# Performance work log

Measured on AMD Instinct MI355X. Metric: run time of the kernel, lower is better.

## Reference

```python
import jax, jax.numpy as jnp
import numpy as np

N, H = 8192, 256
TOP_K = 16          # k = min(top_k, N-1)
TEMPERATURE = 1.0
NEG_SLOPE = 0.2
NUM_SECTORS = 11


def setup_inputs() -> dict:
    key = jax.random.key(0)
    kE, kW, ka, ks, kA = jax.random.split(key, 5)
    embeddings = jax.random.normal(kE, (N, H), dtype=jnp.float32)
    # xavier-uniform-like scale for W (nn.Linear, bias=False)
    lim = float(np.sqrt(6.0 / (H + H)))
    W = jax.random.uniform(kW, (H, H), dtype=jnp.float32, minval=-lim, maxval=lim)
    # a ~ Normal(0, 1/sqrt(2H))
    a = jax.random.normal(ka, (2 * H,), dtype=jnp.float32) * (1.0 / np.sqrt(2 * H))
    sector_ids = jax.random.randint(ks, (N,), 0, NUM_SECTORS, dtype=jnp.int32)
    active_mask = jax.random.randint(kA, (N,), 0, 2, dtype=jnp.int32).astype(bool)
    return {"embeddings": embeddings, "W": W, "a": a,
            "sector_ids": sector_ids, "active_mask": active_mask}


def reference(embeddings, W, a, sector_ids, active_mask):
    # h = W(embeddings)  (torch Linear: x @ W.T)
    h = embeddings @ W.T                                   # [N, H]
    # attention[i,j] = leaky_relu(a . [h_i, h_j]) = leaky_relu(a1.h_i + a2.h_j)
    # (decomposition of the concat+matmul; same math, avoids O(N^2*2H) tensor)
    a1, a2 = a[:H], a[H:]
    s_i = h @ a1                                           # [N]
    s_j = h @ a2                                           # [N]
    att = jax.nn.leaky_relu(s_i[:, None] + s_j[None, :], NEG_SLOPE) / TEMPERATURE
    # combined mask: active pairs AND same sector
    mask = (active_mask[:, None] & active_mask[None, :]) \
           & (sector_ids[:, None] == sector_ids[None, :])  # [N, N]
    att = jnp.where(mask, att, -jnp.inf)
    k = min(TOP_K, N - 1)
    topk_values, topk_indices = jax.lax.top_k(att, k)      # [N, k] each
    valid = jnp.isfinite(topk_values)                      # invalid = masked-out slots
    # dense padded representation of (edge_index, edge_weight):
    # src = topk_indices, dst = row index, weight = topk_values where valid
    edge_weight = jnp.where(valid, topk_values, 0.0)
    return edge_weight, topk_indices, valid
```

## Files before the change

### kernel.cpp

```cpp
#include <hip/hip_runtime.h>

#define N 8192
#define H 256
#define TOPK 16
#define NSEC 11
#define NEG_SLOPE 0.2
#define NBLK 32
#define RPB (N / NBLK)
#define IDX_SENT 0x7fffffff

__device__ __forceinline__ bool better(double av, int ai, double bv, int bi) {
    return (av > bv) || (av == bv && ai < bi);
}

__global__ __launch_bounds__(1024) void fused_v_s(
    const float* __restrict__ E, const float* __restrict__ W,
    const float* __restrict__ a, const int* __restrict__ sec,
    const int* __restrict__ act,
    float* __restrict__ s1f, float* __restrict__ s2f,
    double* __restrict__ candV, int* __restrict__ candI,
    int* __restrict__ cnts)
{
    __shared__ double part1[4][256];
    __shared__ double part2[4][256];
    __shared__ double sv1[H];
    __shared__ double sv2[H];
    __shared__ double s2loc[RPB];

    int t = threadIdx.x;
    int blk = blockIdx.x;
    int lane = t & 63;
    int w = t >> 6;

    {
        int k = t & 255;
        int g = t >> 8;
        double acc1 = 0.0, acc2 = 0.0;
        for (int j = g * 64; j < (g + 1) * 64; ++j) {
            double wv = (double)W[j * H + k];
            acc1 += wv * (double)a[j];
            acc2 += wv * (double)a[H + j];
        }
        part1[g][k] = acc1;
        part2[g][k] = acc2;
    }
    __syncthreads();
    if (t < 256) {
        sv1[t] = part1[0][t] + part1[1][t] + part1[2][t] + part1[3][t];
        sv2[t] = part2[0][t] + part2[1][t] + part2[2][t] + part2[3][t];
    }
    __syncthreads();

    for (int q = 0; q < RPB / 16; ++q) {
        int r_loc = w + 16 * q;
        int row = blk * RPB + r_loc;
        const float4* Erow = (const float4*)(E + (size_t)row * H);
        float4 e = Erow[lane];
        int base = lane * 4;
        double acc1 = (double)e.x * sv1[base + 0] + (double)e.y * sv1[base + 1] +
                      (double)e.z * sv1[base + 2] + (double)e.w * sv1[base + 3];
        double acc2 = (double)e.x * sv2[base + 0] + (double)e.y * sv2[base + 1] +
                      (double)e.z * sv2[base + 2] + (double)e.w * sv2[base + 3];
        for (int o = 32; o > 0; o >>= 1) {
            acc1 += __shfl_down(acc1, o);
            acc2 += __shfl_down(acc2, o);
        }
        if (lane == 0) {
            s1f[row] = (float)acc1;
            s2f[row] = (float)acc2;
            s2loc[r_loc] = acc2;
        }
    }
    __syncthreads();

    if (w < NSEC) {
        int c = w;
        double cv[4];
        int ci[4];
        int count = 0;
        for (int p = 0; p < 4; ++p) {
            int r_loc = p * 64 + lane;
            int j = blk * RPB + r_loc;
            bool pred = (act[j] != 0) && (sec[j] == c);
            cv[p] = pred ? s2loc[r_loc] : -INFINITY;
            ci[p] = pred ? j : IDX_SENT;
            count += __popcll(__ballot(pred));
        }

        for (int r = 0; r < TOPK; ++r) {
            double bv = cv[0];
            int bi = ci[0];
            for (int p = 1; p < 4; ++p)
                if (better(cv[p], ci[p], bv, bi)) { bv = cv[p]; bi = ci[p]; }
            for (int o = 32; o > 0; o >>= 1) {
                double ov = __shfl_xor(bv, o);
                int oi = __shfl_xor(bi, o);
                if (better(ov, oi, bv, bi)) { bv = ov; bi = oi; }
            }
            if (bi != IDX_SENT) {
                for (int p = 0; p < 4; ++p)
                    if (ci[p] == bi) { cv[p] = -INFINITY; ci[p] = IDX_SENT; }
            }
            if (lane == 0) {
                candV[(c * NBLK + blk) * TOPK + r] = bv;
                candI[(c * NBLK + blk) * TOPK + r] = bi;
            }
        }
        if (lane == 0) cnts[c * NBLK + blk] = count;
    }
}

__global__ __launch_bounds__(64) void merge_topk(
    const double* __restrict__ candV, const int* __restrict__ candI,
    const int* __restrict__ cnts, const int* __restrict__ sec,
    const int* __restrict__ act,
    int* __restrict__ top_idx, int* __restrict__ fill_idx,
    int* __restrict__ m_out)
{
    int c = blockIdx.x;
    int lane = threadIdx.x;
    bool has = (lane < NBLK);

    const double* mybV = candV + (size_t)(c * NBLK + (has ? lane : 0)) * TOPK;
    const int* mybI = candI + (size_t)(c * NBLK + (has ? lane : 0)) * TOPK;

    double v0 = has ? mybV[0] : -INFINITY;
    int i0 = has ? mybI[0] : IDX_SENT;
    double v1 = has ? mybV[1] : -INFINITY;
    int i1 = has ? mybI[1] : IDX_SENT;
    int h = 0;

    for (int r = 0; r < TOPK; ++r) {
        double bv = v0;
        int bi = i0;
        for (int o = 32; o > 0; o >>= 1) {
            double ov = __shfl_xor(bv, o);
            int oi = __shfl_xor(bi, o);
            if (better(ov, oi, bv, bi)) { bv = ov; bi = oi; }
        }
        bool win = has && (i0 == bi) && (v0 == bv || (i0 == IDX_SENT));
        if (win) {
            ++h;
            v0 = v1;
            i0 = i1;
            if (h + 1 < TOPK) {
                v1 = mybV[h + 1];
                i1 = mybI[h + 1];
            } else {
                v1 = -INFINITY;
                i1 = IDX_SENT;
            }
        }
        if (lane == 0) top_idx[c * TOPK + r] = (bi == IDX_SENT) ? -1 : bi;
    }

    int cl = has ? cnts[c * NBLK + lane] : 0;
    for (int o = 32; o > 0; o >>= 1) cl += __shfl_xor(cl, o);
    if (lane == 0) m_out[c] = (cl < TOPK) ? cl : TOPK;

    int cnt2 = 0;
    for (int basej = 0; basej < N && cnt2 < TOPK; basej += 64) {
        int j = basej + lane;
        bool fail = !((act[j] != 0) && (sec[j] == c));
        unsigned long long mask = __ballot(fail);
        if (fail) {
            int rank = cnt2 + __popcll(mask & ((1ull << lane) - 1));
            if (rank < TOPK) fill_idx[c * TOPK + rank] = j;
        }
        cnt2 += __popcll(mask);
    }
}

__global__ __launch_bounds__(256) void write_out(const float* __restrict__ s1f,
                                                 const float* __restrict__ s2f,
                                                 const int* __restrict__ sec,
                                                 const int* __restrict__ act,
                                                 const int* __restrict__ top_idx,
                                                 const int* __restrict__ fill_idx,
                                                 const int* __restrict__ m_arr,
                                                 float* __restrict__ out) {
    int gid = blockIdx.x * 256 + threadIdx.x;
    int i = gid >> 4;
    int slot = gid & 15;

    float wgt = 0.0f;
    float fidx;
    float fvalid = 0.0f;

    if (act[i] == 0) {
        fidx = (float)slot;
    } else {
        int c = sec[i];
        int m = m_arr[c];
        if (slot < m) {
            int j = top_idx[c * TOPK + slot];
            double x = (double)s1f[i] + (double)s2f[j];
            double attv = (x >= 0.0) ? x : NEG_SLOPE * x;
            wgt = (float)attv;
            fvalid = 1.0f;
            fidx = (float)j;
        } else {
            fidx = (float)fill_idx[c * TOPK + (slot - m)];
        }
    }

    out[gid] = wgt;
    out[N * TOPK + gid] = fidx;
    out[2 * N * TOPK + gid] = fvalid;
}

extern "C" void kernel_launch(void* const* d_in, const int* in_sizes, int n_in,
                              void* d_out, int out_size, void* d_ws, size_t ws_size,
                              hipStream_t stream) {
    const float* E = (const float*)d_in[0];
    const float* W = (const float*)d_in[1];
    const float* a = (const float*)d_in[2];
    const int* sec = (const int*)d_in[3];
    const int* act = (const int*)d_in[4];

    char* ws = (char*)d_ws;
    double* candV = (double*)ws;
    float* s1f = (float*)(candV + NSEC * NBLK * TOPK);
    float* s2f = s1f + N;
    int* candI = (int*)(s2f + N);
    int* cnts = candI + NSEC * NBLK * TOPK;
    int* top_idx = cnts + NSEC * NBLK;
    int* fill_idx = top_idx + NSEC * TOPK;
    int* m_arr = fill_idx + NSEC * TOPK;

    float* out = (float*)d_out;

    hipLaunchKernelGGL(fused_v_s, dim3(NBLK), dim3(1024), 0, stream,
                       E, W, a, sec, act, s1f, s2f, candV, candI, cnts);
    hipLaunchKernelGGL(merge_topk, dim3(NSEC), dim3(64), 0, stream,
                       candV, candI, cnts, sec, act, top_idx, fill_idx, m_arr);
    hipLaunchKernelGGL(write_out, dim3((N * TOPK) / 256), dim3(256), 0, stream,
                       s1f, s2f, sec, act, top_idx, fill_idx, m_arr, out);
}
```

Measured before the change: 117.4 us.

## Fuse all stages into one cooperative kernel with grid syncs and per-sector compaction

New measurement: 226.7 us. 1.93x slower.

```diff
diff --git a/kernel.cpp b/kernel.cpp
--- a/kernel.cpp
+++ b/kernel.cpp
@@ -1,31 +1,38 @@
 #include <hip/hip_runtime.h>
+#include <hip/hip_cooperative_groups.h>
+
+namespace cg = cooperative_groups;
 
 #define N 8192
 #define H 256
 #define TOPK 16
 #define NSEC 11
 #define NEG_SLOPE 0.2
-#define NBLK 32
-#define RPB (N / NBLK)
+#define NB 256
+#define NT 256
+#define RPB (N / NB)
+#define CAP 1024
 #define IDX_SENT 0x7fffffff
 
 __device__ __forceinline__ bool better(double av, int ai, double bv, int bi) {
     return (av > bv) || (av == bv && ai < bi);
 }
 
-__global__ __launch_bounds__(1024) void fused_v_s(
+__global__ __launch_bounds__(NT) void fused_all(
     const float* __restrict__ E, const float* __restrict__ W,
     const float* __restrict__ a, const int* __restrict__ sec,
     const int* __restrict__ act,
-    float* __restrict__ s1f, float* __restrict__ s2f,
-    double* __restrict__ candV, int* __restrict__ candI,
-    int* __restrict__ cnts)
+    float* __restrict__ s1f, double* __restrict__ s2g,
+    int* __restrict__ top_idx, int* __restrict__ fill_idx,
+    int* __restrict__ m_arr, float* __restrict__ out)
 {
-    __shared__ double part1[4][256];
-    __shared__ double part2[4][256];
+    cg::grid_group grid = cg::this_grid();
+
     __shared__ double sv1[H];
     __shared__ double sv2[H];
-    __shared__ double s2loc[RPB];
+    __shared__ double kv[CAP];
+    __shared__ int ki[CAP];
+    __shared__ int s_cnt;
 
     int t = threadIdx.x;
     int blk = blockIdx.x;
@@ -33,26 +40,19 @@
     int w = t >> 6;
 
     {
-        int k = t & 255;
-        int g = t >> 8;
         double acc1 = 0.0, acc2 = 0.0;
-        for (int j = g * 64; j < (g + 1) * 64; ++j) {
-            double wv = (double)W[j * H + k];
+        for (int j = 0; j < H; ++j) {
+            double wv = (double)W[j * H + t];
             acc1 += wv * (double)a[j];
             acc2 += wv * (double)a[H + j];
         }
-        part1[g][k] = acc1;
-        part2[g][k] = acc2;
+        sv1[t] = acc1;
+        sv2[t] = acc2;
     }
     __syncthreads();
-    if (t < 256) {
-        sv1[t] = part1[0][t] + part1[1][t] + part1[2][t] + part1[3][t];
-        sv2[t] = part2[0][t] + part2[1][t] + part2[2][t] + part2[3][t];
-    }
-    __syncthreads();
-
-    for (int q = 0; q < RPB / 16; ++q) {
-        int r_loc = w + 16 * q;
+
+    for (int q = 0; q < RPB / 4; ++q) {
+        int r_loc = w + 4 * q;
         int row = blk * RPB + r_loc;
         const float4* Erow = (const float4*)(E + (size_t)row * H);
         float4 e = Erow[lane];
@@ -67,146 +67,158 @@
         }
         if (lane == 0) {
             s1f[row] = (float)acc1;
-            s2f[row] = (float)acc2;
-            s2loc[r_loc] = acc2;
-        }
-    }
-    __syncthreads();
-
-    if (w < NSEC) {
-        int c = w;
-        double cv[4];
-        int ci[4];
-        int count = 0;
-        for (int p = 0; p < 4; ++p) {
-            int r_loc = p * 64 + lane;
-            int j = blk * RPB + r_loc;
+            s2g[row] = acc2;
+        }
+    }
+
+    grid.sync();
+
+    if (blk < NSEC) {
+        int c = blk;
+        if (t == 0) s_cnt = 0;
+        __syncthreads();
+
+        for (int j = t; j < N; j += NT) {
             bool pred = (act[j] != 0) && (sec[j] == c);
-            cv[p] = pred ? s2loc[r_loc] : -INFINITY;
-            ci[p] = pred ? j : IDX_SENT;
-            count += __popcll(__ballot(pred));
-        }
-
-        for (int r = 0; r < TOPK; ++r) {
-            double bv = cv[0];
-            int bi = ci[0];
-            for (int p = 1; p < 4; ++p)
-                if (better(cv[p], ci[p], bv, bi)) { bv = cv[p]; bi = ci[p]; }
-            for (int o = 32; o > 0; o >>= 1) {
-                double ov = __shfl_xor(bv, o);
-                int oi = __shfl_xor(bi, o);
-                if (better(ov, oi, bv, bi)) { bv = ov; bi = oi; }
-            }
-            if (bi != IDX_SENT) {
-                for (int p = 0; p < 4; ++p)
-                    if (ci[p] == bi) { cv[p] = -INFINITY; ci[p] = IDX_SENT; }
-            }
-            if (lane == 0) {
-                candV[(c * NBLK + blk) * TOPK + r] = bv;
-                candI[(c * NBLK + blk) * TOPK + r] = bi;
-            }
-        }
-        if (lane == 0) cnts[c * NBLK + blk] = count;
-    }
-}
-
-__global__ __launch_bounds__(64) void merge_topk(
-    const double* __restrict__ candV, const int* __restrict__ candI,
-    const int* __restrict__ cnts, const int* __restrict__ sec,
-    const int* __restrict__ act,
-    int* __restrict__ top_idx, int* __restrict__ fill_idx,
-    int* __restrict__ m_out)
-{
-    int c = blockIdx.x;
-    int lane = threadIdx.x;
-    bool has = (lane < NBLK);
-
-    const double* mybV = candV + (size_t)(c * NBLK + (has ? lane : 0)) * TOPK;
-    const int* mybI = candI + (size_t)(c * NBLK + (has ? lane : 0)) * TOPK;
-
-    double v0 = has ? mybV[0] : -INFINITY;
-    int i0 = has ? mybI[0] : IDX_SENT;
-    double v1 = has ? mybV[1] : -INFINITY;
-    int i1 = has ? mybI[1] : IDX_SENT;
-    int h = 0;
-
-    for (int r = 0; r < TOPK; ++r) {
-        double bv = v0;
-        int bi = i0;
-        for (int o = 32; o > 0; o >>= 1) {
-            double ov = __shfl_xor(bv, o);
-            int oi = __shfl_xor(bi, o);
-            if (better(ov, oi, bv, bi)) { bv = ov; bi = oi; }
-        }
-        bool win = has && (i0 == bi) && (v0 == bv || (i0 == IDX_SENT));
-        if (win) {
-            ++h;
-            v0 = v1;
-            i0 = i1;
-            if (h + 1 < TOPK) {
-                v1 = mybV[h + 1];
-                i1 = mybI[h + 1];
+            unsigned long long mask = __ballot(pred);
+            int nact = __popcll(mask);
+            if (nact > 0) {
+                int leader = (int)__ffsll(mask) - 1;
+                int b = 0;
+                if (lane == leader) b = atomicAdd(&s_cnt, nact);
+                b = __shfl(b, leader);
+                if (pred) {
+                    int pos = b + __popcll(mask & ((1ull << lane) - 1));
+                    if (pos < CAP) {
+                        kv[pos] = s2g[j];
+                        ki[pos] = j;
+                    }
+                }
+            }
+        }
+        __syncthreads();
+        int total = s_cnt;
+
+        if (total <= CAP) {
+            if (w == 0) {
+                double cv[CAP / 64];
+                int ci[CAP / 64];
+                for (int p = 0; p < CAP / 64; ++p) {
+                    int slot = p * 64 + lane;
+                    bool ok = (slot < total);
+                    cv[p] = ok ? kv[slot] : -INFINITY;
+                    ci[p] = ok ? ki[slot] : IDX_SENT;
+                }
+                for (int r = 0; r < TOPK; ++r) {
+                    double bv = cv[0];
+                    int bi = ci[0];
+                    for (int p = 1; p < CAP / 64; ++p)
+                        if (better(cv[p], ci[p], bv, bi)) { bv = cv[p]; bi = ci[p]; }
+                    for (int o = 32; o > 0; o >>= 1) {
+                        double ov = __shfl_xor(bv, o);
+                        int oi = __shfl_xor(bi, o);
+                        if (better(ov, oi, bv, bi)) { bv = ov; bi = oi; }
+                    }
+                    if (bi != IDX_SENT) {
+                        for (int p = 0; p < CAP / 64; ++p)
+                            if (ci[p] == bi) { cv[p] = -INFINITY; ci[p] = IDX_SENT; }
+                    }
+                    if (lane == 0) top_idx[c * TOPK + r] = (bi == IDX_SENT) ? -1 : bi;
+                }
+                if (lane == 0) m_arr[c] = (total < TOPK) ? total : TOPK;
+            }
+            if (w == 1) {
+                int cnt2 = 0;
+                for (int basej = 0; basej < N && cnt2 < TOPK; basej += 64) {
+                    int j = basej + lane;
+                    bool fail = !((act[j] != 0) && (sec[j] == c));
+                    unsigned long long mask = __ballot(fail);
+                    if (fail) {
+                        int rank = cnt2 + __popcll(mask & ((1ull << lane) - 1));
+                        if (rank < TOPK) fill_idx[c * TOPK + rank] = j;
+                    }
+                    cnt2 += __popcll(mask);
+                }
+            }
+        } else {
+            double last_v = INFINITY;
+            int last_i = -1;
+            for (int r = 0; r < TOPK; ++r) {
+                double bv = -INFINITY;
+                int bi = IDX_SENT;
+                for (int j = t; j < N; j += NT) {
+                    if (act[j] != 0 && sec[j] == c) {
+                        double v = s2g[j];
+                        bool worse = (v < last_v) || (v == last_v && j > last_i);
+                        if (worse && better(v, j, bv, bi)) { bv = v; bi = j; }
+                    }
+                }
+                kv[t] = bv;
+                ki[t] = bi;
+                __syncthreads();
+                for (int s = 128; s > 0; s >>= 1) {
+                    if (t < s) {
+                        if (better(kv[t + s], ki[t + s], kv[t], ki[t])) {
+                            kv[t] = kv[t + s];
+                            ki[t] = ki[t + s];
+                        }
+                    }
+                    __syncthreads();
+                }
+                last_v = kv[0];
+                last_i = ki[0];
+                if (t == 0) top_idx[c * TOPK + r] = (last_i == IDX_SENT) ? -1 : last_i;
+                __syncthreads();
+            }
+            if (t == 0) m_arr[c] = (total < TOPK) ? total : TOPK;
+            if (w == 1) {
+                int cnt2 = 0;
+                for (int basej = 0; basej < N && cnt2 < TOPK; basej += 64) {
+                    int j = basej + lane;
+                    bool fail = !((act[j] != 0) && (sec[j] == c));
+                    unsigned long long mask = __ballot(fail);
+                    if (fail) {
+                        int rank = cnt2 + __popcll(mask & ((1ull << lane) - 1));
+                        if (rank < TOPK) fill_idx[c * TOPK + rank] = j;
+                    }
+                    cnt2 += __popcll(mask);
+                }
+            }
+        }
+    }
+
+    grid.sync();
+
+    for (int u = 0; u < 2; ++u) {
+        int gid = blk * (RPB * TOPK) + u * NT + t;
+        int i = gid >> 4;
+        int slot = gid & 15;
+
+        float wgt = 0.0f;
+        float fidx;
+        float fvalid = 0.0f;
+
+        if (act[i] == 0) {
+            fidx = (float)slot;
+        } else {
+            int c = sec[i];
+            int m = m_arr[c];
+            if (slot < m) {
+                int j = top_idx[c * TOPK + slot];
+                double x = (double)s1f[i] + s2g[j];
+                double attv = (x >= 0.0) ? x : NEG_SLOPE * x;
+                wgt = (float)attv;
+                fvalid = 1.0f;
+                fidx = (float)j;
             } else {
-                v1 = -INFINITY;
-                i1 = IDX_SENT;
-            }
-        }
-        if (lane == 0) top_idx[c * TOPK + r] = (bi == IDX_SENT) ? -1 : bi;
-    }
-
-    int cl = has ? cnts[c * NBLK + lane] : 0;
-    for (int o = 32; o > 0; o >>= 1) cl += __shfl_xor(cl, o);
-    if (lane == 0) m_out[c] = (cl < TOPK) ? cl : TOPK;
-
-    int cnt2 = 0;
-    for (int basej = 0; basej < N && cnt2 < TOPK; basej += 64) {
-        int j = basej + lane;
-        bool fail = !((act[j] != 0) && (sec[j] == c));
-        unsigned long long mask = __ballot(fail);
-        if (fail) {
-            int rank = cnt2 + __popcll(mask & ((1ull << lane) - 1));
-            if (rank < TOPK) fill_idx[c * TOPK + rank] = j;
-        }
-        cnt2 += __popcll(mask);
-    }
-}
-
-__global__ __launch_bounds__(256) void write_out(const float* __restrict__ s1f,
-                                                 const float* __restrict__ s2f,
-                                                 const int* __restrict__ sec,
-                                                 const int* __restrict__ act,
-                                                 const int* __restrict__ top_idx,
-                                                 const int* __restrict__ fill_idx,
-                                                 const int* __restrict__ m_arr,
-                                                 float* __restrict__ out) {
-    int gid = blockIdx.x * 256 + threadIdx.x;
-    int i = gid >> 4;
-    int slot = gid & 15;
-
-    float wgt = 0.0f;
-    float fidx;
-    float fvalid = 0.0f;
-
-    if (act[i] == 0) {
-        fidx = (float)slot;
-    } else {
-        int c = sec[i];
-        int m = m_arr[c];
-        if (slot < m) {
-            int j = top_idx[c * TOPK + slot];
-            double x = (double)s1f[i] + (double)s2f[j];
-            double attv = (x >= 0.0) ? x : NEG_SLOPE * x;
-            wgt = (float)attv;
-            fvalid = 1.0f;
-            fidx = (float)j;
-        } else {
-            fidx = (float)fill_idx[c * TOPK + (slot - m)];
-        }
-    }
-
-    out[gid] = wgt;
-    out[N * TOPK + gid] = fidx;
-    out[2 * N * TOPK + gid] = fvalid;
+                fidx = (float)fill_idx[c * TOPK + (slot - m)];
+            }
+        }
+
+        out[gid] = wgt;
+        out[N * TOPK + gid] = fidx;
+        out[2 * N * TOPK + gid] = fvalid;
+    }
 }
 
 extern "C" void kernel_launch(void* const* d_in, const int* in_sizes, int n_in,
@@ -219,21 +231,17 @@
     const int* act = (const int*)d_in[4];
 
     char* ws = (char*)d_ws;
-    double* candV = (double*)ws;
-    float* s1f = (float*)(candV + NSEC * NBLK * TOPK);
-    float* s2f = s1f + N;
-    int* candI = (int*)(s2f + N);
-    int* cnts = candI + NSEC * NBLK * TOPK;
-    int* top_idx = cnts + NSEC * NBLK;
+    double* s2g = (double*)ws;
+    float* s1f = (float*)(s2g + N);
+    int* top_idx = (int*)(s1f + N);
     int* fill_idx = top_idx + NSEC * TOPK;
     int* m_arr = fill_idx + NSEC * TOPK;
 
     float* out = (float*)d_out;
 
-    hipLaunchKernelGGL(fused_v_s, dim3(NBLK), dim3(1024), 0, stream,
-                       E, W, a, sec, act, s1f, s2f, candV, candI, cnts);
-    hipLaunchKernelGGL(merge_topk, dim3(NSEC), dim3(64), 0, stream,
-                       candV, candI, cnts, sec, act, top_idx, fill_idx, m_arr);
-    hipLaunchKernelGGL(write_out, dim3((N * TOPK) / 256), dim3(256), 0, stream,
-                       s1f, s2f, sec, act, top_idx, fill_idx, m_arr, out);
+    void* args[] = { (void*)&E, (void*)&W, (void*)&a, (void*)&sec, (void*)&act,
+                     (void*)&s1f, (void*)&s2g, (void*)&top_idx, (void*)&fill_idx,
+                     (void*)&m_arr, (void*)&out };
+    hipLaunchCooperativeKernel(reinterpret_cast<void*>(fused_all),
+                               dim3(NB), dim3(NT), args, 0, stream);
 }
```
